# Performance work log

Hardware: AMD Instinct MI355X
Metric: run time of the kernel (lower is better)

Reference implementation:

```python
import jax, jax.numpy as jnp
import numpy as np

NUM_HEADS = 16


def setup_inputs() -> dict:
    key = jax.random.key(0)
    k1, k2, k3 = jax.random.split(key, 3)
    B, S, E = 2, 2048, 1024
    hidden_states = jax.random.normal(k1, (B, S, E), dtype=jnp.float32)
    c_attn_w = jax.random.normal(k2, (E, 3 * E), dtype=jnp.float32) * 0.02
    c_attn_b = jnp.zeros((3 * E,), dtype=jnp.float32)
    c_proj_w = jax.random.normal(k3, (E, E), dtype=jnp.float32) * 0.02
    c_proj_b = jnp.zeros((E,), dtype=jnp.float32)
    return {
        "hidden_states": hidden_states,
        "c_attn_w": c_attn_w,
        "c_attn_b": c_attn_b,
        "c_proj_w": c_proj_w,
        "c_proj_b": c_proj_b,
    }


def reference(hidden_states, c_attn_w, c_attn_b, c_proj_w, c_proj_b):
    B, S, E = hidden_states.shape
    H = NUM_HEADS
    D = E // H
    # Conv1D: qkv projection -> [B, S, 3E]
    qkv = jnp.einsum("bse,ef->bsf", hidden_states, c_attn_w) + c_attn_b
    q, k, v = jnp.split(qkv, 3, axis=-1)
    # split heads -> [B, H, S, D]
    def heads(x):
        return x.reshape(B, S, H, D).transpose(0, 2, 1, 3)
    q, k, v = heads(q), heads(k), heads(v)
    # scaled QK^T -> [B, H, S, S]
    scale = jnp.asarray(D, dtype=q.dtype) ** 0.5
    attn_weights = jnp.einsum("bhqd,bhkd->bhqk", q, k) / scale
    # causal mask (bias buffer): True on/below diagonal
    causal = jnp.tril(jnp.ones((S, S), dtype=bool))
    mask_value = jnp.finfo(attn_weights.dtype).min
    attn_weights = jnp.where(causal[None, None, :, :], attn_weights, mask_value)
    attn_weights = jax.nn.softmax(attn_weights, axis=-1)
    # attn @ V -> merge heads -> [B, S, E]
    attn_out = jnp.einsum("bhqk,bhkd->bhqd", attn_weights, v)
    attn_out = attn_out.transpose(0, 2, 1, 3).reshape(B, S, E)
    # output projection (Conv1D)
    out = jnp.einsum("bse,ef->bsf", attn_out, c_proj_w) + c_proj_b
    return out
```

## Files before the change

### kernel.cpp

```cpp
#include <hip/hip_runtime.h>
#include <stdint.h>

typedef __attribute__((ext_vector_type(8))) __bf16 bf16x8;
typedef __attribute__((ext_vector_type(4))) __bf16 bf16x4;
typedef __attribute__((ext_vector_type(4))) float f32x4;

#define MFMA16(a, b, c) __builtin_amdgcn_mfma_f32_16x16x32_bf16(a, b, c, 0, 0, 0)

__device__ __forceinline__ void async_ld16(const __bf16* g, __bf16* lds_base) {
    __builtin_amdgcn_global_load_lds(
        (const __attribute__((address_space(1))) void*)g,
        (__attribute__((address_space(3))) void*)lds_base, 16, 0, 0);
}

__global__ __launch_bounds__(256) void k_prep(
    const float* __restrict__ hs, const float* __restrict__ w1,
    const float* __restrict__ w2, __bf16* __restrict__ hsb,
    __bf16* __restrict__ w1t, __bf16* __restrict__ w2t) {
    __shared__ __bf16 tile[32][33];
    int bid = blockIdx.x, tid = threadIdx.x;
    if (bid < 4096) {
        int i = (bid * 256 + tid) * 4;
        float4 v = *(const float4*)(hs + i);
        bf16x4 o;
        o.x = (__bf16)v.x; o.y = (__bf16)v.y; o.z = (__bf16)v.z; o.w = (__bf16)v.w;
        *(bf16x4*)(hsb + i) = o;
        return;
    }
    const float* in; __bf16* out; int C, tb;
    if (bid < 7168) { in = w1; out = w1t; C = 3072; tb = bid - 4096; }
    else            { in = w2; out = w2t; C = 1024; tb = bid - 7168; }
    const int R = 1024;
    int ntc = C >> 5;
    int c0 = (tb % ntc) * 32, r0 = (tb / ntc) * 32;
    int tx = tid & 31, ty = tid >> 5;
#pragma unroll
    for (int i = 0; i < 4; i++)
        tile[ty + i * 8][tx] = (__bf16)in[(size_t)(r0 + ty + i * 8) * C + c0 + tx];
    __syncthreads();
#pragma unroll
    for (int i = 0; i < 4; i++)
        out[(size_t)(c0 + ty + i * 8) * R + r0 + tx] = tile[tx][ty + i * 8];
}

__global__ __launch_bounds__(256, 3) void k_gemm_qkv(
    const __bf16* __restrict__ A, const __bf16* __restrict__ Bt,
    const float* __restrict__ bias,
    __bf16* __restrict__ Qo, __bf16* __restrict__ Ko, __bf16* __restrict__ Vo) {
    __shared__ __bf16 As[128 * 64];
    __shared__ __bf16 Bs[128 * 64];
    const int Kd = 1024;
    int lid = blockIdx.x;
    int xcd = lid & 7, c = lid >> 3;
    int mi = (xcd >> 1) * 8 + c / 12;
    int ni = (xcd & 1) * 12 + c % 12;
    int n0 = ni * 128, m0 = mi * 128;
    bool tr = (ni < 16);
    int tid = threadIdx.x;
    int wv = tid >> 6, lane = tid & 63;
    int wm = (wv >> 1) * 64, wn = (wv & 1) * 64;
    int quad = lane >> 4, l16 = lane & 15;
    int rl = lane >> 3, sj = lane & 7;
    int sgo = (sj ^ rl) << 3;
    int swl = l16 & 7;
    const __bf16* p0 = tr ? Bs : As;
    const __bf16* p1 = tr ? As : Bs;
    int o0 = tr ? wn : wm, o1 = tr ? wm : wn;
    f32x4 acc[4][4] = {};
    for (int k0 = 0; k0 < Kd; k0 += 64) {
        __syncthreads();
#pragma unroll
        for (int r = 0; r < 4; r++) {
            int row = wv * 32 + r * 8;
            async_ld16(&A[(size_t)(m0 + row + rl) * Kd + k0 + sgo], &As[row * 64]);
            async_ld16(&Bt[(size_t)(n0 + row + rl) * Kd + k0 + sgo], &Bs[row * 64]);
        }
        __syncthreads();
#pragma unroll
        for (int ks = 0; ks < 2; ks++) {
            bf16x8 f0[4], f1[4];
#pragma unroll
            for (int i = 0; i < 4; i++)
                f0[i] = *(const bf16x8*)(
                    &p0[(o0 + i * 16 + l16) * 64 + (((ks * 4 + quad) ^ swl) << 3)]);
#pragma unroll
            for (int j = 0; j < 4; j++)
                f1[j] = *(const bf16x8*)(
                    &p1[(o1 + j * 16 + l16) * 64 + (((ks * 4 + quad) ^ swl) << 3)]);
#pragma unroll
            for (int i = 0; i < 4; i++)
#pragma unroll
                for (int j = 0; j < 4; j++)
                    acc[i][j] = MFMA16(f0[i], f1[j], acc[i][j]);
        }
    }
    if (tr) {
#pragma unroll
        for (int i = 0; i < 4; i++) {
#pragma unroll
            for (int j = 0; j < 4; j++) {
                int nb = n0 + wn + i * 16 + quad * 4;
                int sec = nb >> 10, nl = nb & 1023;
                int h = nl >> 6, d = nl & 63;
                int sg = m0 + wm + j * 16 + l16;
                int bb = sg >> 11, s = sg & 2047;
                f32x4 bv = *(const f32x4*)(&bias[nb]);
                __bf16* dst = (sec == 0) ? Qo : Ko;
                float scl = (sec == 0) ? 0.1803368801f : 1.0f;
                bf16x4 q4;
#pragma unroll
                for (int r = 0; r < 4; r++)
                    q4[r] = (__bf16)((acc[i][j][r] + bv[r]) * scl);
                *(bf16x4*)(&dst[((size_t)(bb * 16 + h) * 2048 + s) * 64 + d]) = q4;
            }
        }
    } else {
#pragma unroll
        for (int i = 0; i < 4; i++) {
#pragma unroll
            for (int j = 0; j < 4; j++) {
                int n = n0 + wn + j * 16 + l16;
                float bv = bias[n];
                int nl = n & 1023;
                int h = nl >> 6, d = nl & 63;
                int mbase = m0 + wm + i * 16 + quad * 4;
                int bb = mbase >> 11, s = mbase & 2047;
                bf16x4 v4;
#pragma unroll
                for (int r = 0; r < 4; r++) v4[r] = (__bf16)(acc[i][j][r] + bv);
                *(bf16x4*)(&Vo[((size_t)(bb * 16 + h) * 64 + d) * 2048 + s]) = v4;
            }
        }
    }
}

__global__ __launch_bounds__(256, 3) void k_gemm_proj(
    const __bf16* __restrict__ A, const __bf16* __restrict__ Bt,
    const float* __restrict__ bias, float* __restrict__ out) {
    __shared__ __bf16 As[64 * 64];
    __shared__ __bf16 Bs[128 * 64];
    const int Kd = 1024;
    int lid = blockIdx.x;
    int xcd = lid & 7, c = lid >> 3;
    int mi = xcd * 8 + (c >> 3);
    int ni = c & 7;
    int n0 = ni * 128, m0 = mi * 64;
    int tid = threadIdx.x;
    int wv = tid >> 6, lane = tid & 63;
    int wm = (wv >> 1) * 32, wn = (wv & 1) * 64;
    int quad = lane >> 4, l16 = lane & 15;
    int rl = lane >> 3, sj = lane & 7;
    int sgo = (sj ^ rl) << 3;
    int swl = l16 & 7;
    f32x4 acc[4][2] = {};
    for (int k0 = 0; k0 < Kd; k0 += 64) {
        __syncthreads();
#pragma unroll
        for (int r = 0; r < 2; r++) {
            int row = wv * 16 + r * 8;
            async_ld16(&A[(size_t)(m0 + row + rl) * Kd + k0 + sgo], &As[row * 64]);
        }
#pragma unroll
        for (int r = 0; r < 4; r++) {
            int row = wv * 32 + r * 8;
            async_ld16(&Bt[(size_t)(n0 + row + rl) * Kd + k0 + sgo], &Bs[row * 64]);
        }
        __syncthreads();
#pragma unroll
        for (int ks = 0; ks < 2; ks++) {
            bf16x8 f0[4], f1[2];
#pragma unroll
            for (int i = 0; i < 4; i++)
                f0[i] = *(const bf16x8*)(
                    &Bs[(wn + i * 16 + l16) * 64 + (((ks * 4 + quad) ^ swl) << 3)]);
#pragma unroll
            for (int j = 0; j < 2; j++)
                f1[j] = *(const bf16x8*)(
                    &As[(wm + j * 16 + l16) * 64 + (((ks * 4 + quad) ^ swl) << 3)]);
#pragma unroll
            for (int i = 0; i < 4; i++)
#pragma unroll
                for (int j = 0; j < 2; j++)
                    acc[i][j] = MFMA16(f0[i], f1[j], acc[i][j]);
        }
    }
#pragma unroll
    for (int i = 0; i < 4; i++) {
#pragma unroll
        for (int j = 0; j < 2; j++) {
            int nb = n0 + wn + i * 16 + quad * 4;
            int m = m0 + wm + j * 16 + l16;
            f32x4 bv = *(const f32x4*)(&bias[nb]);
            f32x4 o = acc[i][j] + bv;
            *(f32x4*)(&out[(size_t)m * 1024 + nb]) = o;
        }
    }
}

__device__ const int ATT_ORDER[24] = {7, 10, 14, 16, 18, 20, 22, 23,
                                      8, 12, 6, 21, 5, 19, 4, 17,
                                      0, 9, 1, 11, 2, 13, 3, 15};

__global__ __launch_bounds__(256, 3) void k_attn(
    const __bf16* __restrict__ Qg, const __bf16* __restrict__ Kg,
    const __bf16* __restrict__ Vtg, __bf16* __restrict__ Op, float* __restrict__ Lp) {
    __shared__ __bf16 Ksb[2][64 * 64];
    __shared__ __bf16 Vtb[2][64 * 64];
    __shared__ __bf16 Ps[128 * 72];
    int bh = blockIdx.x & 31;
    int slot = ATT_ORDER[blockIdx.x >> 5];
    int t, k0, k1;
    if (slot < 8) { t = slot; k0 = 0; k1 = 2 * t + 2; }
    else { int i2 = slot - 8; t = 8 + (i2 >> 1); k0 = (i2 & 1) * 16; k1 = min(k0 + 16, 2 * t + 2); }
    const __bf16* Qp = Qg + (size_t)bh * 2048 * 64;
    const __bf16* Kp = Kg + (size_t)bh * 2048 * 64;
    const __bf16* Vp = Vtg + (size_t)bh * 64 * 2048;
    int tid = threadIdx.x, wv = tid >> 6, lane = tid & 63;
    int quad = lane >> 4, l16 = lane & 15;
    int rl = lane >> 3, sj = lane & 7;
    int sgo = (sj ^ rl) << 3;
    int swl = l16 & 7;

    bf16x8 qf[2][2];
#pragma unroll
    for (int qn = 0; qn < 2; qn++)
#pragma unroll
        for (int ks = 0; ks < 2; ks++)
            qf[qn][ks] = *(const bf16x8*)(
                &Qp[(size_t)(t * 128 + wv * 32 + qn * 16 + l16) * 64 + ks * 32 + quad * 8]);
    const f32x4 zf = {0.f, 0.f, 0.f, 0.f};
    f32x4 lacc[2] = {zf, zf};
    f32x4 acc_o[2][4] = {};
    int qwmax = t * 128 + wv * 32 + 31;

    auto stage = [&](int buf, int kt) {
#pragma unroll
        for (int half = 0; half < 2; half++) {
            int r0 = wv * 16 + half * 8;
            async_ld16(&Kp[(size_t)(kt * 64 + r0 + rl) * 64 + sgo], &Ksb[buf][r0 * 64]);
            async_ld16(&Vp[(size_t)(r0 + rl) * 2048 + kt * 64 + sgo], &Vtb[buf][r0 * 64]);
        }
    };

    stage(0, k0);
    __syncthreads();

    for (int kt = k0; kt < k1; kt++) {
        int cur = (kt - k0) & 1;
        if (kt + 1 < k1) stage(cur ^ 1, kt + 1);
        if (kt * 64 <= qwmax) {
            const __bf16* Kc = Ksb[cur];
            const __bf16* Vc = Vtb[cur];
            f32x4 s[2][4];
#pragma unroll
            for (int ks = 0; ks < 2; ks++) {
                bf16x8 kf[4];
#pragma unroll
                for (int i = 0; i < 4; i++)
                    kf[i] = *(const bf16x8*)(
                        &Kc[(i * 16 + l16) * 64 + (((ks * 4 + quad) ^ swl) << 3)]);
                __builtin_amdgcn_s_setprio(1);
#pragma unroll
                for (int i = 0; i < 4; i++)
#pragma unroll
                    for (int qn = 0; qn < 2; qn++)
                        s[qn][i] = MFMA16(kf[i], qf[qn][ks], ks == 0 ? zf : s[qn][i]);
                __builtin_amdgcn_s_setprio(0);
            }
#pragma unroll
            for (int qn = 0; qn < 2; qn++) {
                int qmin = t * 128 + wv * 32 + qn * 16;
                if (kt * 64 + 63 > qmin) {
#pragma unroll
                    for (int i = 0; i < 4; i++)
#pragma unroll
                        for (int r = 0; r < 4; r++)
                            if (kt * 64 + i * 16 + quad * 4 + r > qmin + l16) s[qn][i][r] = -1e30f;
                }
            }
#pragma unroll
            for (int qn = 0; qn < 2; qn++)
#pragma unroll
                for (int i = 0; i < 4; i++) {
                    f32x4 pe;
#pragma unroll
                    for (int r = 0; r < 4; r++) pe[r] = exp2f(s[qn][i][r]);
                    lacc[qn] += pe;
                    bf16x4 pk;
#pragma unroll
                    for (int r = 0; r < 4; r++) pk[r] = (__bf16)pe[r];
                    *(bf16x4*)(&Ps[(wv * 32 + qn * 16 + l16) * 72 + i * 16 + quad * 4]) = pk;
                }
#pragma unroll
            for (int ks = 0; ks < 2; ks++) {
                bf16x8 pf[2];
#pragma unroll
                for (int qn = 0; qn < 2; qn++)
                    pf[qn] = *(const bf16x8*)(
                        &Ps[(wv * 32 + qn * 16 + l16) * 72 + ks * 32 + quad * 8]);
                bf16x8 vf[4];
#pragma unroll
                for (int i = 0; i < 4; i++)
                    vf[i] = *(const bf16x8*)(
                        &Vc[(i * 16 + l16) * 64 + (((ks * 4 + quad) ^ swl) << 3)]);
                __builtin_amdgcn_s_setprio(1);
#pragma unroll
                for (int i = 0; i < 4; i++)
#pragma unroll
                    for (int qn = 0; qn < 2; qn++)
                        acc_o[qn][i] = MFMA16(vf[i], pf[qn], acc_o[qn][i]);
                __builtin_amdgcn_s_setprio(0);
            }
        }
        __syncthreads();
    }
    size_t pbase = (size_t)slot * 32 + bh;
#pragma unroll
    for (int qn = 0; qn < 2; qn++) {
        float ls = lacc[qn][0] + lacc[qn][1] + lacc[qn][2] + lacc[qn][3];
        ls += __shfl_xor(ls, 16);
        ls += __shfl_xor(ls, 32);
        int ql = wv * 32 + qn * 16 + l16;
        if (quad == 0) Lp[pbase * 128 + ql] = ls;
#pragma unroll
        for (int i = 0; i < 4; i++) {
            bf16x4 o4;
#pragma unroll
            for (int r = 0; r < 4; r++) o4[r] = (__bf16)acc_o[qn][i][r];
            *(bf16x4*)(&Op[(pbase * 128 + ql) * 64 + i * 16 + quad * 4]) = o4;
        }
    }
}

__global__ __launch_bounds__(256) void k_attn_combine(
    const __bf16* __restrict__ Op, const float* __restrict__ Lp,
    __bf16* __restrict__ AOb) {
    int gid = blockIdx.x * 256 + threadIdx.x;
    int d4 = gid & 15;
    int q = (gid >> 4) & 2047;
    int bh = gid >> 15;
    int t = q >> 7, ql = q & 127;
    int n = (t <= 7) ? 1 : 2;
    int base = (t <= 7) ? t : 8 + 2 * (t - 8);
    float L = 0.f, o[4] = {};
    for (int c = 0; c < n; c++) {
        size_t idx = (size_t)(base + c) * 32 + bh;
        L += Lp[idx * 128 + ql];
        bf16x4 p4 = *(const bf16x4*)(&Op[(idx * 128 + ql) * 64 + d4 * 4]);
#pragma unroll
        for (int r = 0; r < 4; r++) o[r] += (float)p4[r];
    }
    float inv = 1.f / L;
    int b = bh >> 4, h = bh & 15;
    bf16x4 o4;
#pragma unroll
    for (int r = 0; r < 4; r++) o4[r] = (__bf16)(o[r] * inv);
    *(bf16x4*)(&AOb[((size_t)b * 2048 + q) * 1024 + h * 64 + d4 * 4]) = o4;
}

extern "C" void kernel_launch(void* const* d_in, const int* in_sizes, int n_in,
                              void* d_out, int out_size, void* d_ws, size_t ws_size,
                              hipStream_t stream) {
    const float* hs = (const float*)d_in[0];
    const float* w1 = (const float*)d_in[1];
    const float* b1 = (const float*)d_in[2];
    const float* w2 = (const float*)d_in[3];
    const float* b2 = (const float*)d_in[4];
    float* out = (float*)d_out;

    char* ws = (char*)d_ws;
    __bf16* hsb = (__bf16*)(ws);
    __bf16* w1t = (__bf16*)(ws + (size_t)8 * 1024 * 1024);
    __bf16* w2t = (__bf16*)(ws + (size_t)14 * 1024 * 1024);
    __bf16* Qb  = (__bf16*)(ws + (size_t)16 * 1024 * 1024);
    __bf16* Kb  = (__bf16*)(ws + (size_t)24 * 1024 * 1024);
    __bf16* Vb  = (__bf16*)(ws + (size_t)32 * 1024 * 1024);
    __bf16* AOb = (__bf16*)(ws + (size_t)40 * 1024 * 1024);
    __bf16* Opart = (__bf16*)(ws);
    float*  Lpart = (float*)(ws + (size_t)13 * 1024 * 1024);

    k_prep<<<8192, 256, 0, stream>>>(hs, w1, w2, hsb, w1t, w2t);
    k_gemm_qkv<<<768, 256, 0, stream>>>(hsb, w1t, b1, Qb, Kb, Vb);
    k_attn<<<768, 256, 0, stream>>>(Qb, Kb, Vb, Opart, Lpart);
    k_attn_combine<<<4096, 256, 0, stream>>>(Opart, Lpart, AOb);
    k_gemm_proj<<<512, 256, 0, stream>>>(AOb, w2t, b2, out);
}
```

Measured before the change: 176.5 us.

## Split attention into 8-tile KV chunks and cut LDS to raise occupancy

Attention work is re-partitioned into 40 slots per batch-head, each covering up to 8 KV tiles, with tables ordering slots longest-first. The combine kernel gains a per-query-tile slot list and can merge up to four partials. K is single-buffered in LDS with its next-tile load issued after a mid-iteration barrier, and the padded P buffer becomes an XOR-swizzled unpadded one. Together these shrink LDS so four blocks fit per CU instead of three. The costs are more partial outputs to write and combine, an extra barrier per KV tile, and a reworked workspace layout.

```diff
diff --git a/kernel.cpp b/kernel.cpp
--- a/kernel.cpp
+++ b/kernel.cpp
@@ -197,21 +197,23 @@
     }
 }
 
-__device__ const int ATT_ORDER[24] = {7, 10, 14, 16, 18, 20, 22, 23,
-                                      8, 12, 6, 21, 5, 19, 4, 17,
-                                      0, 9, 1, 11, 2, 13, 3, 15};
-
-__global__ __launch_bounds__(256, 3) void k_attn(
+__device__ const int T_OF[40] = {15,15,15,15, 14,14,14, 13,13,13, 12,12,12,
+                                 11,11,11, 10,10, 9,9, 8,8, 7,7, 6, 5, 4, 3,
+                                 14,10,6,2, 13,9,5,1, 12,8,4,0};
+__device__ const int K0_OF[40] = {0,8,16,24, 0,8,16, 0,8,16, 0,8,16,
+                                  0,8,16, 0,8, 0,8, 0,8, 0,8, 0, 0, 0, 0,
+                                  24,16,8,0, 24,16,8,0, 24,16,8,0};
+
+__global__ __launch_bounds__(256, 4) void k_attn(
     const __bf16* __restrict__ Qg, const __bf16* __restrict__ Kg,
     const __bf16* __restrict__ Vtg, __bf16* __restrict__ Op, float* __restrict__ Lp) {
-    __shared__ __bf16 Ksb[2][64 * 64];
+    __shared__ __bf16 Ksb[64 * 64];
     __shared__ __bf16 Vtb[2][64 * 64];
-    __shared__ __bf16 Ps[128 * 72];
+    __shared__ __bf16 Ps[128 * 64];
     int bh = blockIdx.x & 31;
-    int slot = ATT_ORDER[blockIdx.x >> 5];
-    int t, k0, k1;
-    if (slot < 8) { t = slot; k0 = 0; k1 = 2 * t + 2; }
-    else { int i2 = slot - 8; t = 8 + (i2 >> 1); k0 = (i2 & 1) * 16; k1 = min(k0 + 16, 2 * t + 2); }
+    int slot = blockIdx.x >> 5;
+    int t = T_OF[slot], k0 = K0_OF[slot];
+    int k1 = min(k0 + 8, 2 * t + 2);
     const __bf16* Qp = Qg + (size_t)bh * 2048 * 64;
     const __bf16* Kp = Kg + (size_t)bh * 2048 * 64;
     const __bf16* Vp = Vtg + (size_t)bh * 64 * 2048;
@@ -232,25 +234,28 @@
     f32x4 lacc[2] = {zf, zf};
     f32x4 acc_o[2][4] = {};
     int qwmax = t * 128 + wv * 32 + 31;
-
-    auto stage = [&](int buf, int kt) {
-#pragma unroll
-        for (int half = 0; half < 2; half++) {
-            int r0 = wv * 16 + half * 8;
-            async_ld16(&Kp[(size_t)(kt * 64 + r0 + rl) * 64 + sgo], &Ksb[buf][r0 * 64]);
-            async_ld16(&Vp[(size_t)(r0 + rl) * 2048 + kt * 64 + sgo], &Vtb[buf][r0 * 64]);
-        }
-    };
-
-    stage(0, k0);
+    int qrow[2] = {wv * 32 + l16, wv * 32 + 16 + l16};
+
+#pragma unroll
+    for (int half = 0; half < 2; half++) {
+        int r0 = wv * 16 + half * 8;
+        async_ld16(&Kp[(size_t)(k0 * 64 + r0 + rl) * 64 + sgo], &Ksb[r0 * 64]);
+        async_ld16(&Vp[(size_t)(r0 + rl) * 2048 + k0 * 64 + sgo], &Vtb[0][r0 * 64]);
+    }
     __syncthreads();
 
     for (int kt = k0; kt < k1; kt++) {
         int cur = (kt - k0) & 1;
-        if (kt + 1 < k1) stage(cur ^ 1, kt + 1);
-        if (kt * 64 <= qwmax) {
-            const __bf16* Kc = Ksb[cur];
-            const __bf16* Vc = Vtb[cur];
+        if (kt + 1 < k1) {
+#pragma unroll
+            for (int half = 0; half < 2; half++) {
+                int r0 = wv * 16 + half * 8;
+                async_ld16(&Vp[(size_t)(r0 + rl) * 2048 + (kt + 1) * 64 + sgo],
+                           &Vtb[cur ^ 1][r0 * 64]);
+            }
+        }
+        bool active = (kt * 64 <= qwmax);
+        if (active) {
             f32x4 s[2][4];
 #pragma unroll
             for (int ks = 0; ks < 2; ks++) {
@@ -258,7 +263,7 @@
 #pragma unroll
                 for (int i = 0; i < 4; i++)
                     kf[i] = *(const bf16x8*)(
-                        &Kc[(i * 16 + l16) * 64 + (((ks * 4 + quad) ^ swl) << 3)]);
+                        &Ksb[(i * 16 + l16) * 64 + (((ks * 4 + quad) ^ swl) << 3)]);
                 __builtin_amdgcn_s_setprio(1);
 #pragma unroll
                 for (int i = 0; i < 4; i++)
@@ -289,15 +294,28 @@
                     bf16x4 pk;
 #pragma unroll
                     for (int r = 0; r < 4; r++) pk[r] = (__bf16)pe[r];
-                    *(bf16x4*)(&Ps[(wv * 32 + qn * 16 + l16) * 72 + i * 16 + quad * 4]) = pk;
+                    *(bf16x4*)(&Ps[qrow[qn] * 64 +
+                                   (((i * 4 + quad) ^ (swl << 1)) << 2)]) = pk;
                 }
+        }
+        __syncthreads();
+        if (kt + 1 < k1) {
+#pragma unroll
+            for (int half = 0; half < 2; half++) {
+                int r0 = wv * 16 + half * 8;
+                async_ld16(&Kp[(size_t)((kt + 1) * 64 + r0 + rl) * 64 + sgo],
+                           &Ksb[r0 * 64]);
+            }
+        }
+        if (active) {
+            const __bf16* Vc = Vtb[cur];
 #pragma unroll
             for (int ks = 0; ks < 2; ks++) {
                 bf16x8 pf[2];
 #pragma unroll
                 for (int qn = 0; qn < 2; qn++)
                     pf[qn] = *(const bf16x8*)(
-                        &Ps[(wv * 32 + qn * 16 + l16) * 72 + ks * 32 + quad * 8]);
+                        &Ps[qrow[qn] * 64 + (((ks * 4 + quad) ^ swl) << 3)]);
                 bf16x8 vf[4];
 #pragma unroll
                 for (int i = 0; i < 4; i++)
@@ -331,6 +349,13 @@
         }
     }
 }
+
+__device__ const int CCNT[16] = {1,1,1,1,2,2,2,2,3,3,3,3,4,4,4,4};
+__device__ const int CSLOT[64] = {
+    39,0,0,0,  35,0,0,0,  31,0,0,0,  27,0,0,0,
+    26,38,0,0, 25,34,0,0, 24,30,0,0, 22,23,0,0,
+    20,21,37,0, 18,19,33,0, 16,17,29,0, 13,14,15,0,
+    10,11,12,36, 7,8,9,32, 4,5,6,28, 0,1,2,3};
 
 __global__ __launch_bounds__(256) void k_attn_combine(
     const __bf16* __restrict__ Op, const float* __restrict__ Lp,
@@ -340,11 +365,10 @@
     int q = (gid >> 4) & 2047;
     int bh = gid >> 15;
     int t = q >> 7, ql = q & 127;
-    int n = (t <= 7) ? 1 : 2;
-    int base = (t <= 7) ? t : 8 + 2 * (t - 8);
+    int n = CCNT[t];
     float L = 0.f, o[4] = {};
     for (int c = 0; c < n; c++) {
-        size_t idx = (size_t)(base + c) * 32 + bh;
+        size_t idx = (size_t)CSLOT[t * 4 + c] * 32 + bh;
         L += Lp[idx * 128 + ql];
         bf16x4 p4 = *(const bf16x4*)(&Op[(idx * 128 + ql) * 64 + d4 * 4]);
 #pragma unroll
@@ -368,20 +392,21 @@
     const float* b2 = (const float*)d_in[4];
     float* out = (float*)d_out;
 
+    const size_t MB = 1024 * 1024;
     char* ws = (char*)d_ws;
-    __bf16* hsb = (__bf16*)(ws);
-    __bf16* w1t = (__bf16*)(ws + (size_t)8 * 1024 * 1024);
-    __bf16* w2t = (__bf16*)(ws + (size_t)14 * 1024 * 1024);
-    __bf16* Qb  = (__bf16*)(ws + (size_t)16 * 1024 * 1024);
-    __bf16* Kb  = (__bf16*)(ws + (size_t)24 * 1024 * 1024);
-    __bf16* Vb  = (__bf16*)(ws + (size_t)32 * 1024 * 1024);
-    __bf16* AOb = (__bf16*)(ws + (size_t)40 * 1024 * 1024);
-    __bf16* Opart = (__bf16*)(ws);
-    float*  Lpart = (float*)(ws + (size_t)13 * 1024 * 1024);
+    __bf16* w2t = (__bf16*)(ws);
+    __bf16* Qb  = (__bf16*)(ws + 2 * MB);
+    __bf16* Kb  = (__bf16*)(ws + 10 * MB);
+    __bf16* Vb  = (__bf16*)(ws + 18 * MB);
+    __bf16* hsb = (__bf16*)(ws + 26 * MB);
+    __bf16* w1t = (__bf16*)(ws + 34 * MB);
+    __bf16* Opart = (__bf16*)(ws + 26 * MB);
+    float*  Lpart = (float*)(ws + 26 * MB + (size_t)40 * 32 * 128 * 64 * 2);
+    __bf16* AOb = (__bf16*)(ws + 2 * MB);
 
     k_prep<<<8192, 256, 0, stream>>>(hs, w1, w2, hsb, w1t, w2t);
     k_gemm_qkv<<<768, 256, 0, stream>>>(hsb, w1t, b1, Qb, Kb, Vb);
-    k_attn<<<768, 256, 0, stream>>>(Qb, Kb, Vb, Opart, Lpart);
+    k_attn<<<1280, 256, 0, stream>>>(Qb, Kb, Vb, Opart, Lpart);
     k_attn_combine<<<4096, 256, 0, stream>>>(Opart, Lpart, AOb);
     k_gemm_proj<<<512, 256, 0, stream>>>(AOb, w2t, b2, out);
 }
```

New measurement: 231.1 us. 1.31x slower.
